# Kernel optimization log

Hardware: AMD Instinct MI355X
Metric: run time of the kernel (lower is better)

## Reference

```python
import jax, jax.numpy as jnp
import numpy as np

EPS = 1e-12


def setup_inputs() -> dict:
    key = jax.random.key(0)
    k1, k2, k3, k4 = jax.random.split(key, 4)
    N, H, W, D, K = 64, 32, 32, 512, 64
    x = jax.random.normal(k1, (N, H, W, D), dtype=jnp.float32)
    W_assign = jax.random.normal(k2, (D, K), dtype=jnp.float32) * 0.05  # 1x1 conv kernel
    b_assign = jax.random.normal(k3, (K,), dtype=jnp.float32) * 0.05
    C = jax.random.normal(k4, (D, K), dtype=jnp.float32) * 0.05  # cluster centers
    return {"x": x, "W_assign": W_assign, "b_assign": b_assign, "C": C}


def _l2norm(v, axis):
    return v / jnp.sqrt(jnp.sum(v * v, axis=axis, keepdims=True) + EPS)


def reference(x, W_assign, b_assign, C):
    # 1x1 conv = matmul over channel dim: [N,H,W,D] @ [D,K] -> [N,H,W,K]
    s = jnp.einsum('nhwd,dk->nhwk', x, W_assign) + b_assign
    a = jax.nn.softmax(s, axis=-1)                       # soft assignment over K
    # VLAD: v[n,d,k] = sum_hw a[n,h,w,k] * (x[n,h,w,d] + C[d,k])
    # reformulated as two small contractions (no [N,H,W,D,K] intermediate):
    v = jnp.einsum('nhwd,nhwk->ndk', x, a)               # feature-weighted sums
    a_sum = jnp.sum(a, axis=(1, 2))                      # [N,K]
    v = v + a_sum[:, None, :] * C[None, :, :]            # [N,D,K]
    # intra-normalization: L2 over D per cluster (after transpose to [N,K,D])
    v = _l2norm(jnp.transpose(v, (0, 2, 1)), axis=-1)    # [N,K,D]
    v = jnp.transpose(v, (0, 2, 1))                      # [N,D,K]
    # flatten and final L2 normalize -> [N, D*K]
    v = v.reshape(v.shape[0], -1)
    return _l2norm(v, axis=-1)
```

## Files before the change

kernel.cpp:

```cpp
#include <hip/hip_runtime.h>


#define EPSF 1e-12f

typedef short bf16x8 __attribute__((ext_vector_type(8)));
typedef float f32x16 __attribute__((ext_vector_type(16)));

__device__ inline unsigned short f2bf_rne(float f) {
  union { float f; unsigned u; } v; v.f = f;
  unsigned u = v.u;
  unsigned r = u + 0x7fffu + ((u >> 16) & 1u);
  return (unsigned short)(r >> 16);
}
__device__ inline unsigned pk2(float a, float b) {
#if __has_builtin(__builtin_amdgcn_cvt_pk_bf16_f32)
  auto r = __builtin_amdgcn_cvt_pk_bf16_f32(a, b);
  return __builtin_bit_cast(unsigned, r);
#else
  return (unsigned)f2bf_rne(a) | ((unsigned)f2bf_rne(b) << 16);
#endif
}
__device__ inline bf16x8 pack8(float4 lo, float4 hi) {
  union { unsigned u[4]; bf16x8 v; } r;
  r.u[0] = pk2(lo.x, lo.y);
  r.u[1] = pk2(lo.z, lo.w);
  r.u[2] = pk2(hi.x, hi.y);
  r.u[3] = pk2(hi.z, hi.w);
  return r.v;
}

__global__ __launch_bounds__(256) void kprep(
    const float* __restrict__ Wm, unsigned short* __restrict__ wt,
    float* __restrict__ stats ) {
  const int t = threadIdx.x, bx = blockIdx.x;
  if (bx == 8) {
    float4 z = {0.f, 0.f, 0.f, 0.f};
#pragma unroll
    for (int r = 0; r < 8; ++r)
      *(float4*)&stats[(size_t)(r * 256 + t) * 4] = z;
    return;
  }
  __shared__ float tile[64][65];
  {
    int col = (t & 15) * 4, rbase = t >> 4;
#pragma unroll
    for (int r = 0; r < 4; ++r) {
      int row = rbase + 16 * r;
      *(float4*)&tile[row][col] =
          *(const float4*)&Wm[(size_t)(bx * 64 + row) * 64 + col];
    }
  }
  __syncthreads();
  int k = t >> 2, seg = (t & 3) * 16;
  size_t o = (size_t)k * 512 + bx * 64 + seg;
#pragma unroll
  for (int j = 0; j < 16; j += 2)
    *(unsigned*)&wt[o + j] = pk2(tile[seg + j][k], tile[seg + j + 1][k]);
}

__global__ __launch_bounds__(256) void kassign(
    const float* __restrict__ x, const unsigned short* __restrict__ wt,
    const float* __restrict__ b, unsigned short* __restrict__ at,
    float* __restrict__ a_sum) {
  const int t = threadIdx.x;
  const int w = t >> 6, lane = t & 63, l31 = lane & 31, h = lane >> 5;
  const int bx = blockIdx.x;
  const int n = bx >> 3;
  const int hwbase = (bx & 7) * 128 + 32 * w;
  const size_t prow = (size_t)(bx * 128 + 32 * w + l31) * 512;
  const unsigned short* w0 = wt + (size_t)l31 * 512;
  const unsigned short* w1 = wt + (size_t)(32 + l31) * 512;

  f32x16 acc0, acc1;
#pragma unroll
  for (int i = 0; i < 16; ++i) { acc0[i] = 0.f; acc1[i] = 0.f; }

#pragma unroll 8
  for (int st = 0; st < 32; ++st) {
    const int kd = st * 16 + h * 8;
    float4 xa = *(const float4*)&x[prow + kd];
    float4 xb = *(const float4*)&x[prow + kd + 4];
    bf16x8 ax = pack8(xa, xb);
    bf16x8 b0 = *(const bf16x8*)&w0[kd];
    bf16x8 b1 = *(const bf16x8*)&w1[kd];
    acc0 = __builtin_amdgcn_mfma_f32_32x32x16_bf16(ax, b0, acc0, 0, 0, 0);
    acc1 = __builtin_amdgcn_mfma_f32_32x32x16_bf16(ax, b1, acc1, 0, 0, 0);
  }

  const float bias0 = b[l31], bias1 = b[32 + l31];
  float a0[16], a1[16];
  float sum0 = 0.f, sum1 = 0.f;
#pragma unroll
  for (int r = 0; r < 16; ++r) {
    float s0 = acc0[r] + bias0, s1 = acc1[r] + bias1;
    float m = fmaxf(s0, s1);
#pragma unroll
    for (int msk = 1; msk < 32; msk <<= 1) m = fmaxf(m, __shfl_xor(m, msk, 64));
    float e0 = __expf(s0 - m), e1 = __expf(s1 - m);
    float S = e0 + e1;
#pragma unroll
    for (int msk = 1; msk < 32; msk <<= 1) S += __shfl_xor(S, msk, 64);
    float inv = 1.0f / S;
    a0[r] = e0 * inv; a1[r] = e1 * inv;
    sum0 += a0[r]; sum1 += a1[r];
  }
  const int hwb = hwbase + 4 * h;
  const size_t kb0 = ((size_t)n * 64 + l31) * 1024;
  const size_t kb1 = ((size_t)n * 64 + 32 + l31) * 1024;
#pragma unroll
  for (int g = 0; g < 4; ++g) {
    int hw = hwb + 8 * g;
    uint2 u;
    u.x = pk2(a0[4 * g + 0], a0[4 * g + 1]);
    u.y = pk2(a0[4 * g + 2], a0[4 * g + 3]);
    *(uint2*)&at[kb0 + hw] = u;
    u.x = pk2(a1[4 * g + 0], a1[4 * g + 1]);
    u.y = pk2(a1[4 * g + 2], a1[4 * g + 3]);
    *(uint2*)&at[kb1 + hw] = u;
  }
  sum0 += __shfl_xor(sum0, 32, 64);
  sum1 += __shfl_xor(sum1, 32, 64);
  if (lane < 32) {
    atomicAdd(&a_sum[n * 64 + l31], sum0);
    atomicAdd(&a_sum[n * 64 + 32 + l31], sum1);
  }
}

__global__ __launch_bounds__(256) void kvlad(
    const float* __restrict__ x, const unsigned short* __restrict__ at,
    const float* __restrict__ a_sum, const float* __restrict__ C,
    float* __restrict__ out, float* __restrict__ ssq) {
  const int t = threadIdx.x;
  const int w = t >> 6, lane = t & 63, l31 = lane & 31, h = lane >> 5;
  const int n = blockIdx.y, d0 = blockIdx.x * 64;
  const int dw = 32 * (w & 1), kw = 32 * (w >> 1);
  const int d = d0 + dw + l31;
  const float* xl = x + (size_t)n * 524288 + d;
  const unsigned short* al = at + ((size_t)n * 64 + kw + l31) * 1024;

  f32x16 acc;
#pragma unroll
  for (int i = 0; i < 16; ++i) acc[i] = 0.f;

#pragma unroll 4
  for (int m = 0; m < 64; ++m) {
    const int hwb = m * 16 + h * 8;
    float a[8];
#pragma unroll
    for (int j = 0; j < 8; ++j) a[j] = xl[(size_t)(hwb + j) * 512];
    union { unsigned u[4]; bf16x8 v; } ax;
    ax.u[0] = pk2(a[0], a[1]);
    ax.u[1] = pk2(a[2], a[3]);
    ax.u[2] = pk2(a[4], a[5]);
    ax.u[3] = pk2(a[6], a[7]);
    bf16x8 bb = *(const bf16x8*)&al[hwb];
    acc = __builtin_amdgcn_mfma_f32_32x32x16_bf16(ax.v, bb, acc, 0, 0, 0);
  }

  const int k = kw + l31;
  const float as = a_sum[n * 64 + k];
  float sq = 0.f;
#pragma unroll
  for (int r = 0; r < 16; ++r) {
    int row = (r & 3) + 8 * (r >> 2) + 4 * h;
    int dd = d0 + dw + row;
    float o = acc[r] + as * C[(size_t)dd * 64 + k];
    out[((size_t)n * 512 + dd) * 64 + k] = o;
    sq += o * o;
  }
  atomicAdd(&ssq[n * 64 + k], sq);
}

__global__ __launch_bounds__(256) void kscale(
    float* __restrict__ out, const float* __restrict__ ssq) {
  const int n = blockIdx.y, slice = blockIdx.x;
  const int t = threadIdx.x, k = t & 63, rg = t >> 6;
  __shared__ float sk[64];
  __shared__ float tot;
  if (t < 64) {
    float c = ssq[n * 64 + t];
    sk[t] = rsqrtf(c + EPSF);
    float contrib = c / (c + EPSF);
#pragma unroll
    for (int m = 32; m; m >>= 1) contrib += __shfl_xor(contrib, m, 64);
    if (t == 0) tot = rsqrtf(contrib + EPSF);
  }
  __syncthreads();
  const float scale = sk[k] * tot;
  float* vb = out + (size_t)n * 32768 + (size_t)slice * 4096;
#pragma unroll
  for (int r = rg; r < 64; r += 4) vb[r * 64 + k] *= scale;
}

extern "C" void kernel_launch(void* const* d_in, const int* in_sizes, int n_in,
                              void* d_out, int out_size, void* d_ws, size_t ws_size,
                              hipStream_t stream) {
  const float* x  = (const float*)d_in[0];
  const float* Wm = (const float*)d_in[1];
  const float* b  = (const float*)d_in[2];
  const float* C  = (const float*)d_in[3];
  float* out = (float*)d_out;

  unsigned short* at = (unsigned short*)d_ws;
  unsigned short* wt = at + (size_t)64 * 64 * 1024;
  float* stats = (float*)(wt + (size_t)64 * 512);
  float* a_sum = stats;
  float* ssq   = stats + 4096;

  kprep<<<dim3(9), dim3(256), 0, stream>>>(Wm, wt, stats);
  kassign<<<dim3(512), dim3(256), 0, stream>>>(x, wt, b, at, a_sum);
  kvlad<<<dim3(8, 64), dim3(256), 0, stream>>>(x, at, a_sum, C, out, ssq);
  kscale<<<dim3(8, 64), dim3(256), 0, stream>>>(out, ssq);
}
```

Measured before the change: 245.3 us.

## Stage x rows through swizzled LDS in kassign and reorder kvlad block mapping

kassign now loads x with coalesced float4 reads across lanes, one row per half-wave. It converts the values to bf16 and writes them into a per-wave, XOR-swizzled LDS tile in 128-column chunks. MFMA A-fragments are then read from LDS, replacing the previous strided per-lane row reads from global memory. kvlad uses a 1D grid with the batch index in the low bits, so concurrently running blocks share the same d-slice, which is meant to improve L2 locality. The LDS tile uses 64KB per block, which may limit occupancy, and the code relies on wave-local ordering with no explicit barrier.

```diff
diff --git a/kernel.cpp b/kernel.cpp
--- a/kernel.cpp
+++ b/kernel.cpp
@@ -19,14 +19,6 @@
 #else
   return (unsigned)f2bf_rne(a) | ((unsigned)f2bf_rne(b) << 16);
 #endif
-}
-__device__ inline bf16x8 pack8(float4 lo, float4 hi) {
-  union { unsigned u[4]; bf16x8 v; } r;
-  r.u[0] = pk2(lo.x, lo.y);
-  r.u[1] = pk2(lo.z, lo.w);
-  r.u[2] = pk2(hi.x, hi.y);
-  r.u[3] = pk2(hi.z, hi.w);
-  return r.v;
 }
 
 __global__ __launch_bounds__(256) void kprep(
@@ -67,24 +59,41 @@
   const int bx = blockIdx.x;
   const int n = bx >> 3;
   const int hwbase = (bx & 7) * 128 + 32 * w;
-  const size_t prow = (size_t)(bx * 128 + 32 * w + l31) * 512;
+  const size_t rowbase = (size_t)(bx * 128 + 32 * w);
   const unsigned short* w0 = wt + (size_t)l31 * 512;
   const unsigned short* w1 = wt + (size_t)(32 + l31) * 512;
 
+  __shared__ unsigned short lds[4][2][4096];
+  unsigned short (*tile)[4096] = lds[w];
+
   f32x16 acc0, acc1;
 #pragma unroll
   for (int i = 0; i < 16; ++i) { acc0[i] = 0.f; acc1[i] = 0.f; }
 
-#pragma unroll 8
-  for (int st = 0; st < 32; ++st) {
-    const int kd = st * 16 + h * 8;
-    float4 xa = *(const float4*)&x[prow + kd];
-    float4 xb = *(const float4*)&x[prow + kd + 4];
-    bf16x8 ax = pack8(xa, xb);
-    bf16x8 b0 = *(const bf16x8*)&w0[kd];
-    bf16x8 b1 = *(const bf16x8*)&w1[kd];
-    acc0 = __builtin_amdgcn_mfma_f32_32x32x16_bf16(ax, b0, acc0, 0, 0, 0);
-    acc1 = __builtin_amdgcn_mfma_f32_32x32x16_bf16(ax, b1, acc1, 0, 0, 0);
+#pragma unroll
+  for (int q = 0; q < 4; ++q) {
+    const int buf = q & 1;
+    const int dbase = q * 128;
+#pragma unroll
+    for (int j = 0; j < 16; ++j) {
+      const int r = 2 * j + h;
+      float4 v = *(const float4*)&x[(rowbase + r) * 512 + dbase + 4 * l31];
+      uint2 u;
+      u.x = pk2(v.x, v.y);
+      u.y = pk2(v.z, v.w);
+      const int idx = (r * 128 + 4 * l31) ^ (8 * (r & 7));
+      *(uint2*)&tile[buf][idx] = u;
+    }
+#pragma unroll
+    for (int stl = 0; stl < 8; ++stl) {
+      const int kd = dbase + stl * 16 + h * 8;
+      const int ridx = (l31 * 128 + 16 * stl + 8 * h) ^ (8 * (l31 & 7));
+      bf16x8 ax = *(const bf16x8*)&tile[buf][ridx];
+      bf16x8 b0 = *(const bf16x8*)&w0[kd];
+      bf16x8 b1 = *(const bf16x8*)&w1[kd];
+      acc0 = __builtin_amdgcn_mfma_f32_32x32x16_bf16(ax, b0, acc0, 0, 0, 0);
+      acc1 = __builtin_amdgcn_mfma_f32_32x32x16_bf16(ax, b1, acc1, 0, 0, 0);
+    }
   }
 
   const float bias0 = b[l31], bias1 = b[32 + l31];
@@ -132,7 +141,8 @@
     float* __restrict__ out, float* __restrict__ ssq) {
   const int t = threadIdx.x;
   const int w = t >> 6, lane = t & 63, l31 = lane & 31, h = lane >> 5;
-  const int n = blockIdx.y, d0 = blockIdx.x * 64;
+  const int bid = blockIdx.x;
+  const int n = bid & 63, d0 = (bid >> 6) * 64;
   const int dw = 32 * (w & 1), kw = 32 * (w >> 1);
   const int d = d0 + dw + l31;
   const float* xl = x + (size_t)n * 524288 + d;
@@ -209,6 +219,6 @@
 
   kprep<<<dim3(9), dim3(256), 0, stream>>>(Wm, wt, stats);
   kassign<<<dim3(512), dim3(256), 0, stream>>>(x, wt, b, at, a_sum);
-  kvlad<<<dim3(8, 64), dim3(256), 0, stream>>>(x, at, a_sum, C, out, ssq);
+  kvlad<<<dim3(512), dim3(256), 0, stream>>>(x, at, a_sum, C, out, ssq);
   kscale<<<dim3(8, 64), dim3(256), 0, stream>>>(out, ssq);
 }
```

Measured after the change: 243.3 us. About the same (-0.8%).

## Fuse soft-assignment and VLAD contraction into one kernel with LDS staging

Applied to the files above, without the earlier changes.

Merges the assignment GEMM/softmax kernel and the VLAD aggregation kernel into one kernel. Each block stages bf16 x tiles (transposed, XOR-swizzled) and soft assignments in LDS, so x is read from global memory once instead of twice. Each of 4 pixel chunks per image writes a partial [D,K] result, and a new post kernel sums the partials and adds the a_sum*C term. The cost is 256 blocks at one block per CU with a large LDS footprint, scattered 2-byte LDS transpose stores, and extra partial-buffer traffic.

```diff
diff --git a/kernel.cpp b/kernel.cpp
--- a/kernel.cpp
+++ b/kernel.cpp
@@ -20,14 +20,6 @@
   return (unsigned)f2bf_rne(a) | ((unsigned)f2bf_rne(b) << 16);
 #endif
 }
-__device__ inline bf16x8 pack8(float4 lo, float4 hi) {
-  union { unsigned u[4]; bf16x8 v; } r;
-  r.u[0] = pk2(lo.x, lo.y);
-  r.u[1] = pk2(lo.z, lo.w);
-  r.u[2] = pk2(hi.x, hi.y);
-  r.u[3] = pk2(hi.z, hi.w);
-  return r.v;
-}
 
 __global__ __launch_bounds__(256) void kprep(
     const float* __restrict__ Wm, unsigned short* __restrict__ wt,
@@ -58,114 +50,146 @@
     *(unsigned*)&wt[o + j] = pk2(tile[seg + j][k], tile[seg + j + 1][k]);
 }
 
-__global__ __launch_bounds__(256) void kassign(
+__global__ __launch_bounds__(256, 1) void kfused(
     const float* __restrict__ x, const unsigned short* __restrict__ wt,
-    const float* __restrict__ b, unsigned short* __restrict__ at,
+    const float* __restrict__ b, float* __restrict__ vpart,
     float* __restrict__ a_sum) {
+  __shared__ unsigned short xbT[512 * 128];
+  __shared__ unsigned short ab[64 * 128];
   const int t = threadIdx.x;
   const int w = t >> 6, lane = t & 63, l31 = lane & 31, h = lane >> 5;
-  const int bx = blockIdx.x;
-  const int n = bx >> 3;
-  const int hwbase = (bx & 7) * 128 + 32 * w;
-  const size_t prow = (size_t)(bx * 128 + 32 * w + l31) * 512;
+  const int bid = blockIdx.x;
+  const int n = bid >> 2, c = bid & 3;
   const unsigned short* w0 = wt + (size_t)l31 * 512;
   const unsigned short* w1 = wt + (size_t)(32 + l31) * 512;
-
-  f32x16 acc0, acc1;
-#pragma unroll
-  for (int i = 0; i < 16; ++i) { acc0[i] = 0.f; acc1[i] = 0.f; }
-
+  const float bias0 = b[l31], bias1 = b[32 + l31];
+  const int colpx = w * 32 + l31;
+
+  f32x16 accv[8];
+#pragma unroll
+  for (int i = 0; i < 8; ++i)
+#pragma unroll
+    for (int j = 0; j < 16; ++j) accv[i][j] = 0.f;
+
+  float asum0 = 0.f, asum1 = 0.f;
+
+  for (int s = 0; s < 2; ++s) {
+    const int pxb = c * 256 + s * 128;
+    const float* rowp = x + ((size_t)n * 1024 + pxb + colpx) * 512;
+    f32x16 s0, s1;
+#pragma unroll
+    for (int i = 0; i < 16; ++i) { s0[i] = 0.f; s1[i] = 0.f; }
 #pragma unroll 8
-  for (int st = 0; st < 32; ++st) {
-    const int kd = st * 16 + h * 8;
-    float4 xa = *(const float4*)&x[prow + kd];
-    float4 xb = *(const float4*)&x[prow + kd + 4];
-    bf16x8 ax = pack8(xa, xb);
-    bf16x8 b0 = *(const bf16x8*)&w0[kd];
-    bf16x8 b1 = *(const bf16x8*)&w1[kd];
-    acc0 = __builtin_amdgcn_mfma_f32_32x32x16_bf16(ax, b0, acc0, 0, 0, 0);
-    acc1 = __builtin_amdgcn_mfma_f32_32x32x16_bf16(ax, b1, acc1, 0, 0, 0);
-  }
-
-  const float bias0 = b[l31], bias1 = b[32 + l31];
-  float a0[16], a1[16];
-  float sum0 = 0.f, sum1 = 0.f;
+    for (int st = 0; st < 32; ++st) {
+      const int kd = st * 16 + h * 8;
+      float4 xa = *(const float4*)&rowp[kd];
+      float4 xb = *(const float4*)&rowp[kd + 4];
+      union { unsigned u[4]; bf16x8 v; } ax;
+      ax.u[0] = pk2(xa.x, xa.y);
+      ax.u[1] = pk2(xa.z, xa.w);
+      ax.u[2] = pk2(xb.x, xb.y);
+      ax.u[3] = pk2(xb.z, xb.w);
+      bf16x8 b0 = *(const bf16x8*)&w0[kd];
+      bf16x8 b1 = *(const bf16x8*)&w1[kd];
+      s0 = __builtin_amdgcn_mfma_f32_32x32x16_bf16(ax.v, b0, s0, 0, 0, 0);
+      s1 = __builtin_amdgcn_mfma_f32_32x32x16_bf16(ax.v, b1, s1, 0, 0, 0);
+#pragma unroll
+      for (int j2 = 0; j2 < 4; ++j2) {
+        const int da = kd + 2 * j2, db = da + 1;
+        xbT[da * 128 + (colpx ^ ((da & 15) << 3))] =
+            (unsigned short)(ax.u[j2] & 0xffffu);
+        xbT[db * 128 + (colpx ^ ((db & 15) << 3))] =
+            (unsigned short)(ax.u[j2] >> 16);
+      }
+    }
+    float a0[16], a1[16];
+    float sum0 = 0.f, sum1 = 0.f;
+#pragma unroll
+    for (int r = 0; r < 16; ++r) {
+      float v0 = s0[r] + bias0, v1 = s1[r] + bias1;
+      float m = fmaxf(v0, v1);
+#pragma unroll
+      for (int msk = 1; msk < 32; msk <<= 1)
+        m = fmaxf(m, __shfl_xor(m, msk, 64));
+      float e0 = __expf(v0 - m), e1 = __expf(v1 - m);
+      float S = e0 + e1;
+#pragma unroll
+      for (int msk = 1; msk < 32; msk <<= 1) S += __shfl_xor(S, msk, 64);
+      float inv = 1.0f / S;
+      a0[r] = e0 * inv; a1[r] = e1 * inv;
+      sum0 += a0[r]; sum1 += a1[r];
+    }
+    asum0 += sum0; asum1 += sum1;
+#pragma unroll
+    for (int g = 0; g < 4; ++g) {
+      const int cb = w * 32 + 8 * g + 4 * h;
+      uint2 uu;
+      uu.x = pk2(a0[4 * g + 0], a0[4 * g + 1]);
+      uu.y = pk2(a0[4 * g + 2], a0[4 * g + 3]);
+      *(uint2*)&ab[l31 * 128 + (cb ^ ((l31 & 15) << 3))] = uu;
+      uu.x = pk2(a1[4 * g + 0], a1[4 * g + 1]);
+      uu.y = pk2(a1[4 * g + 2], a1[4 * g + 3]);
+      *(uint2*)&ab[(32 + l31) * 128 + (cb ^ ((l31 & 15) << 3))] = uu;
+    }
+    __syncthreads();
+    const int dw = w * 128;
+#pragma unroll
+    for (int s8 = 0; s8 < 8; ++s8) {
+      const int px0 = s8 * 16 + 8 * h;
+      bf16x8 bb0 = *(const bf16x8*)&ab[l31 * 128 + (px0 ^ ((l31 & 15) << 3))];
+      bf16x8 bb1 =
+          *(const bf16x8*)&ab[(32 + l31) * 128 + (px0 ^ ((l31 & 15) << 3))];
+#pragma unroll
+      for (int dt = 0; dt < 4; ++dt) {
+        const int dr = dw + dt * 32 + l31;
+        bf16x8 aa = *(const bf16x8*)&xbT[dr * 128 + (px0 ^ ((dr & 15) << 3))];
+        accv[dt * 2 + 0] =
+            __builtin_amdgcn_mfma_f32_32x32x16_bf16(aa, bb0, accv[dt * 2 + 0], 0, 0, 0);
+        accv[dt * 2 + 1] =
+            __builtin_amdgcn_mfma_f32_32x32x16_bf16(aa, bb1, accv[dt * 2 + 1], 0, 0, 0);
+      }
+    }
+    __syncthreads();
+  }
+  asum0 += __shfl_xor(asum0, 32, 64);
+  asum1 += __shfl_xor(asum1, 32, 64);
+  if (lane < 32) {
+    atomicAdd(&a_sum[n * 64 + l31], asum0);
+    atomicAdd(&a_sum[n * 64 + 32 + l31], asum1);
+  }
+  float* vp = vpart + (size_t)c * 2097152 + (size_t)n * 32768;
+#pragma unroll
+  for (int dt = 0; dt < 4; ++dt) {
+#pragma unroll
+    for (int kt = 0; kt < 2; ++kt) {
+      const f32x16 a = accv[dt * 2 + kt];
+      const int kcol = kt * 32 + l31;
+#pragma unroll
+      for (int r = 0; r < 16; ++r) {
+        const int drow = w * 128 + dt * 32 + (r & 3) + 8 * (r >> 2) + 4 * h;
+        vp[drow * 64 + kcol] = a[r];
+      }
+    }
+  }
+}
+
+__global__ __launch_bounds__(256) void kpost(
+    const float* __restrict__ vpart, const float* __restrict__ a_sum,
+    const float* __restrict__ C, float* __restrict__ out,
+    float* __restrict__ ssq) {
+  const int bid = blockIdx.x;
+  const int n = bid & 63, d0 = (bid >> 6) * 64;
+  const int t = threadIdx.x, k = t & 63, dr = t >> 6;
+  const float as = a_sum[n * 64 + k];
+  const size_t nb = (size_t)n * 32768;
+  float sq = 0.f;
 #pragma unroll
   for (int r = 0; r < 16; ++r) {
-    float s0 = acc0[r] + bias0, s1 = acc1[r] + bias1;
-    float m = fmaxf(s0, s1);
-#pragma unroll
-    for (int msk = 1; msk < 32; msk <<= 1) m = fmaxf(m, __shfl_xor(m, msk, 64));
-    float e0 = __expf(s0 - m), e1 = __expf(s1 - m);
-    float S = e0 + e1;
-#pragma unroll
-    for (int msk = 1; msk < 32; msk <<= 1) S += __shfl_xor(S, msk, 64);
-    float inv = 1.0f / S;
-    a0[r] = e0 * inv; a1[r] = e1 * inv;
-    sum0 += a0[r]; sum1 += a1[r];
-  }
-  const int hwb = hwbase + 4 * h;
-  const size_t kb0 = ((size_t)n * 64 + l31) * 1024;
-  const size_t kb1 = ((size_t)n * 64 + 32 + l31) * 1024;
-#pragma unroll
-  for (int g = 0; g < 4; ++g) {
-    int hw = hwb + 8 * g;
-    uint2 u;
-    u.x = pk2(a0[4 * g + 0], a0[4 * g + 1]);
-    u.y = pk2(a0[4 * g + 2], a0[4 * g + 3]);
-    *(uint2*)&at[kb0 + hw] = u;
-    u.x = pk2(a1[4 * g + 0], a1[4 * g + 1]);
-    u.y = pk2(a1[4 * g + 2], a1[4 * g + 3]);
-    *(uint2*)&at[kb1 + hw] = u;
-  }
-  sum0 += __shfl_xor(sum0, 32, 64);
-  sum1 += __shfl_xor(sum1, 32, 64);
-  if (lane < 32) {
-    atomicAdd(&a_sum[n * 64 + l31], sum0);
-    atomicAdd(&a_sum[n * 64 + 32 + l31], sum1);
-  }
-}
-
-__global__ __launch_bounds__(256) void kvlad(
-    const float* __restrict__ x, const unsigned short* __restrict__ at,
-    const float* __restrict__ a_sum, const float* __restrict__ C,
-    float* __restrict__ out, float* __restrict__ ssq) {
-  const int t = threadIdx.x;
-  const int w = t >> 6, lane = t & 63, l31 = lane & 31, h = lane >> 5;
-  const int n = blockIdx.y, d0 = blockIdx.x * 64;
-  const int dw = 32 * (w & 1), kw = 32 * (w >> 1);
-  const int d = d0 + dw + l31;
-  const float* xl = x + (size_t)n * 524288 + d;
-  const unsigned short* al = at + ((size_t)n * 64 + kw + l31) * 1024;
-
-  f32x16 acc;
-#pragma unroll
-  for (int i = 0; i < 16; ++i) acc[i] = 0.f;
-
-#pragma unroll 4
-  for (int m = 0; m < 64; ++m) {
-    const int hwb = m * 16 + h * 8;
-    float a[8];
-#pragma unroll
-    for (int j = 0; j < 8; ++j) a[j] = xl[(size_t)(hwb + j) * 512];
-    union { unsigned u[4]; bf16x8 v; } ax;
-    ax.u[0] = pk2(a[0], a[1]);
-    ax.u[1] = pk2(a[2], a[3]);
-    ax.u[2] = pk2(a[4], a[5]);
-    ax.u[3] = pk2(a[6], a[7]);
-    bf16x8 bb = *(const bf16x8*)&al[hwb];
-    acc = __builtin_amdgcn_mfma_f32_32x32x16_bf16(ax.v, bb, acc, 0, 0, 0);
-  }
-
-  const int k = kw + l31;
-  const float as = a_sum[n * 64 + k];
-  float sq = 0.f;
-#pragma unroll
-  for (int r = 0; r < 16; ++r) {
-    int row = (r & 3) + 8 * (r >> 2) + 4 * h;
-    int dd = d0 + dw + row;
-    float o = acc[r] + as * C[(size_t)dd * 64 + k];
-    out[((size_t)n * 512 + dd) * 64 + k] = o;
+    const int d = d0 + dr * 16 + r;
+    const size_t idx = nb + (size_t)d * 64 + k;
+    float o = vpart[idx] + vpart[idx + 2097152] + vpart[idx + 4194304] +
+              vpart[idx + 6291456] + as * C[(size_t)d * 64 + k];
+    out[idx] = o;
     sq += o * o;
   }
   atomicAdd(&ssq[n * 64 + k], sq);
@@ -178,9 +202,9 @@
   __shared__ float sk[64];
   __shared__ float tot;
   if (t < 64) {
-    float c = ssq[n * 64 + t];
-    sk[t] = rsqrtf(c + EPSF);
-    float contrib = c / (c + EPSF);
+    float cc = ssq[n * 64 + t];
+    sk[t] = rsqrtf(cc + EPSF);
+    float contrib = cc / (cc + EPSF);
 #pragma unroll
     for (int m = 32; m; m >>= 1) contrib += __shfl_xor(contrib, m, 64);
     if (t == 0) tot = rsqrtf(contrib + EPSF);
@@ -201,14 +225,14 @@
   const float* C  = (const float*)d_in[3];
   float* out = (float*)d_out;
 
-  unsigned short* at = (unsigned short*)d_ws;
-  unsigned short* wt = at + (size_t)64 * 64 * 1024;
+  float* vpart = (float*)d_ws;
+  unsigned short* wt = (unsigned short*)(vpart + 4 * 2097152);
   float* stats = (float*)(wt + (size_t)64 * 512);
   float* a_sum = stats;
   float* ssq   = stats + 4096;
 
   kprep<<<dim3(9), dim3(256), 0, stream>>>(Wm, wt, stats);
-  kassign<<<dim3(512), dim3(256), 0, stream>>>(x, wt, b, at, a_sum);
-  kvlad<<<dim3(8, 64), dim3(256), 0, stream>>>(x, at, a_sum, C, out, ssq);
+  kfused<<<dim3(256), dim3(256), 0, stream>>>(x, wt, b, vpart, a_sum);
+  kpost<<<dim3(512), dim3(256), 0, stream>>>(vpart, a_sum, C, out, ssq);
   kscale<<<dim3(8, 64), dim3(256), 0, stream>>>(out, ssq);
 }
```

Result: faster. 231.3 us (-5.7%).
